# Kernel optimization log

Measured on AMD Instinct MI355X. Metric: run time of the kernel, lower is better.

Reference implementation:

```python
import jax, jax.numpy as jnp
import numpy as np

EPS = 1e-5  # BatchNorm eps

def gcn_conv(x, src, dst, n, W, b):
    # PyG GCNConv (normalize=True, add_self_loops=True):
    # out = D^{-1/2} (A + I) D^{-1/2} X W + b, messages aggregated at target (dst)
    deg = jax.ops.segment_sum(jnp.ones_like(dst, dtype=x.dtype), dst, num_segments=n)
    dinv = jnp.where(deg > 0, jax.lax.rsqrt(deg), 0.0)
    norm = dinv[src] * dinv[dst]                      # [E+N]
    xw = x @ W                                        # [N, out]
    out = jax.ops.segment_sum(norm[:, None] * xw[src], dst, num_segments=n)
    return out + b

def batch_norm(x, gamma, beta):
    # training-mode BatchNorm1d over node dim, biased variance
    mean = jnp.mean(x, axis=0)
    var = jnp.mean(jnp.square(x - mean), axis=0)
    return gamma * (x - mean) * jax.lax.rsqrt(var + EPS) + beta

def setup_inputs() -> dict:
    key = jax.random.key(0)
    ks = jax.random.split(key, 12)
    N, E, F_IN, DIM, F_OUT, L = 200000, 6400000, 64, 16, 16, 4
    x = jax.random.normal(ks[0], (N, F_IN), dtype=jnp.float32)
    edge_index = jax.random.randint(ks[1], (2, E), 0, N, dtype=jnp.int64)
    s = 0.1
    return {
        "x": x,
        "edge_index": edge_index,
        "W_in": jax.random.normal(ks[2], (F_IN, DIM), jnp.float32) * s,
        "b_in": jnp.zeros((DIM,), jnp.float32),
        "Ws": jax.random.normal(ks[3], (L, DIM, DIM), jnp.float32) * s,
        "bs": jnp.zeros((L, DIM), jnp.float32),
        "gammas": jnp.ones((L, DIM), jnp.float32),
        "betas": jnp.zeros((L, DIM), jnp.float32),
        "W_sin": jax.random.normal(ks[4], (DIM, F_OUT), jnp.float32) * s,
        "b_sin": jnp.zeros((F_OUT,), jnp.float32),
        "W_cos": jax.random.normal(ks[5], (DIM, F_OUT), jnp.float32) * s,
        "b_cos": jnp.zeros((F_OUT,), jnp.float32),
    }

def reference(x, edge_index, W_in, b_in, Ws, bs, gammas, betas, W_sin, b_sin, W_cos, b_cos):
    n = x.shape[0]
    loops = jnp.arange(n, dtype=edge_index.dtype)
    src = jnp.concatenate([edge_index[0], loops])   # add self loops once
    dst = jnp.concatenate([edge_index[1], loops])
    h = gcn_conv(x, src, dst, n, W_in, b_in)
    for l in range(Ws.shape[0]):
        h = gcn_conv(h, src, dst, n, Ws[l], bs[l])
        h = jax.nn.relu(batch_norm(h, gammas[l], betas[l]))
    sin_out = jax.nn.relu(gcn_conv(h, src, dst, n, W_sin, b_sin))
    cos_out = jax.nn.relu(gcn_conv(h, src, dst, n, W_cos, b_cos))
    return (sin_out, cos_out)
```

## Files before the change

kernel.cpp:

```cpp
#include <hip/hip_runtime.h>
#include <hip/hip_fp16.h>


#define DIM 16
#define F_IN 64
#define BUCK_SHIFT 10
#define BUCK_SIZE 1024
#define MAXB 256
#define HIST_CHUNK 4096
#define BIN_CHUNK 4096
#define EPB 16
#define CSR_CAP 33280

#define WA_OFF 0
#define WB_OFF 272
#define BA_OFF 544
#define BB_OFF 560
#define SW_SIZE 576
#define WIDX(f, j) ((f) * 17 + (j))


__global__ void hist_kernel(const int* __restrict__ dst, int* __restrict__ ghist,
                            int E, int nb) {
    __shared__ int lh[MAXB];
    int t = threadIdx.x;
    for (int i = t; i < nb; i += 256) lh[i] = 0;
    __syncthreads();
    int base = blockIdx.x * HIST_CHUNK;
    int end = min(base + HIST_CHUNK, E);
    for (int e = base + t; e < end; e += 256) atomicAdd(&lh[dst[e] >> BUCK_SHIFT], 1);
    __syncthreads();
    for (int b = t; b < nb; b += 256) {
        int c = lh[b];
        if (c) atomicAdd(&ghist[b], c);
    }
}

__global__ void scan_kernel(const int* __restrict__ ghist, int* __restrict__ boff,
                            int* __restrict__ cursor, int nb, int E) {
    __shared__ int sd[256];
    int t = threadIdx.x;
    int v = (t < nb) ? ghist[t] : 0;
    sd[t] = v;
    __syncthreads();
    for (int off = 1; off < 256; off <<= 1) {
        int u = (t >= off) ? sd[t - off] : 0;
        __syncthreads();
        sd[t] += u;
        __syncthreads();
    }
    if (t < nb) {
        int excl = sd[t] - v;
        boff[t] = excl;
        cursor[t] = excl;
    }
    if (t == 255) boff[nb] = E;
}

__launch_bounds__(256)
__global__ void bin_kernel(const int* __restrict__ src, const int* __restrict__ dst,
                           int* __restrict__ cursor, unsigned* __restrict__ packed,
                           int E, int nb) {
    __shared__ unsigned sedge[BIN_CHUNK];
    __shared__ unsigned char sbid[BIN_CHUNK];
    __shared__ int lh[MAXB];
    __shared__ int sd[MAXB];
    __shared__ int lstart[MAXB];
    __shared__ int lrank[MAXB];
    __shared__ int gbase[MAXB];

    int t = threadIdx.x;
    int base = blockIdx.x * BIN_CHUNK;
    int end = min(base + BIN_CHUNK, E);
    lh[t] = 0;
    __syncthreads();

    unsigned pv[EPB];
    int bk[EPB];
#pragma unroll
    for (int i = 0; i < EPB; ++i) {
        int e = base + t + i * 256;
        if (e < end) {
            int d = dst[e];
            int b = d >> BUCK_SHIFT;
            pv[i] = (unsigned)src[e] | ((unsigned)(d & (BUCK_SIZE - 1)) << 18);
            bk[i] = b;
            atomicAdd(&lh[b], 1);
        } else {
            bk[i] = -1;
            pv[i] = 0u;
        }
    }
    __syncthreads();

    int v = (t < nb) ? lh[t] : 0;
    sd[t] = v;
    __syncthreads();
    for (int off = 1; off < 256; off <<= 1) {
        int u = (t >= off) ? sd[t - off] : 0;
        __syncthreads();
        sd[t] += u;
        __syncthreads();
    }
    if (t < nb) {
        lstart[t] = sd[t] - v;
        lrank[t] = 0;
        gbase[t] = v ? atomicAdd(&cursor[t], v) : 0;
    }
    __syncthreads();

#pragma unroll
    for (int i = 0; i < EPB; ++i) {
        int b = bk[i];
        if (b >= 0) {
            int rank = atomicAdd(&lrank[b], 1);
            int p = lstart[b] + rank;
            sedge[p] = pv[i];
            sbid[p] = (unsigned char)b;
        }
    }
    __syncthreads();

    int total = end - base;
    for (int j = t; j < total; j += 256) {
        int b = sbid[j];
        packed[(size_t)gbase[b] + (unsigned)(j - lstart[b])] = sedge[j];
    }
}

__launch_bounds__(1024)
__global__ void csr_kernel(const unsigned* __restrict__ packed, const int* __restrict__ boff,
                           int* __restrict__ rowptr, float* __restrict__ dinv,
                           int* __restrict__ col, int N, int E) {
    extern __shared__ unsigned smem[];
    unsigned* sstage = smem;
    int* sd   = (int*)smem;
    int* cnt  = (int*)(smem + CSR_CAP);
    int* scur = cnt + BUCK_SIZE;

    int t = threadIdx.x, blk = blockIdx.x;
    cnt[t] = 0;
    __syncthreads();
    int b0 = boff[blk], e1 = boff[blk + 1];
    for (int e = b0 + t; e < e1; e += 1024) atomicAdd(&cnt[packed[e] >> 18], 1);
    __syncthreads();
    int d = cnt[t];
    sd[t] = d;
    __syncthreads();
    for (int off = 1; off < 1024; off <<= 1) {
        int v = (t >= off) ? sd[t - off] : 0;
        __syncthreads();
        sd[t] += v;
        __syncthreads();
    }
    int lstart = sd[t] - d;
    int i = (blk << BUCK_SHIFT) + t;
    if (i < N) {
        rowptr[i] = b0 + lstart;
        dinv[i] = rsqrtf((float)(d + 1));
        if (i == N - 1) rowptr[N] = E;
    }
    scur[t] = lstart;
    __syncthreads();
    for (int e = b0 + t; e < e1; e += 1024) {
        unsigned k = packed[e];
        int pos = atomicAdd(&scur[k >> 18], 1);
        unsigned val = k & 0x3FFFFu;
        if (pos < CSR_CAP) sstage[pos] = val;
        else col[(size_t)b0 + pos] = val;
    }
    __syncthreads();
    int total = e1 - b0;
    int lim = min(total, CSR_CAP);
    for (int j = t; j < lim; j += 1024) col[(size_t)b0 + j] = sstage[j];
}


__global__ void z0_kernel(const float* __restrict__ x, const float* __restrict__ W,
                          const float* __restrict__ dinv,
                          __half* __restrict__ z, int n) {
    __shared__ float sW[F_IN * DIM];
    int t = threadIdx.x;
#pragma unroll
    for (int j = 0; j < 4; ++j) sW[t + j * 256] = W[t + j * 256];
    __syncthreads();
    int idx = blockIdx.x * 256 + t;
    if (idx >= n * 2) return;
    int node = idx >> 1, p = idx & 1;
    float acc[8] = {0, 0, 0, 0, 0, 0, 0, 0};
    const float4* xr = (const float4*)(x + (size_t)node * F_IN);
#pragma unroll
    for (int k4 = 0; k4 < 16; ++k4) {
        float4 xv = xr[k4];
        float c[4] = { xv.x, xv.y, xv.z, xv.w };
#pragma unroll
        for (int cc = 0; cc < 4; ++cc) {
            const float* wr = &sW[(k4 * 4 + cc) * DIM + p * 8];
#pragma unroll
            for (int j = 0; j < 8; ++j) acc[j] += c[cc] * wr[j];
        }
    }
    float di = dinv[node];
    __half2 o[4];
#pragma unroll
    for (int m = 0; m < 4; ++m) o[m] = __floats2half2_rn(di * acc[2 * m], di * acc[2 * m + 1]);
    *(float4*)(z + ((size_t)node << 4) + p * 8) = *(float4*)o;
}

#define ACC_ROW(vl, vh)                                                        \
    {                                                                          \
        const __half2* hl_ = (const __half2*)&(vl);                            \
        const __half2* hh_ = (const __half2*)&(vh);                            \
        _Pragma("unroll")                                                      \
        for (int m_ = 0; m_ < 4; ++m_) {                                       \
            float2 f2_ = __half22float2(hl_[m_]);                              \
            a[2 * m_] += f2_.x; a[2 * m_ + 1] += f2_.y;                        \
            float2 g2_ = __half22float2(hh_[m_]);                              \
            a[8 + 2 * m_] += g2_.x; a[8 + 2 * m_ + 1] += g2_.y;                \
        }                                                                      \
    }


template <int MODE>
__launch_bounds__(256)
__global__ void gatherF_kernel(const int* __restrict__ rowptr, const int* __restrict__ col,
                               const __half* __restrict__ z, const float* __restrict__ dinv,
                               const float* __restrict__ Wa, const float* __restrict__ Wb,
                               const float* __restrict__ ba, const float* __restrict__ bb,
                               float* __restrict__ o1, float* __restrict__ o2,
                               __half* __restrict__ znext, float* __restrict__ bnsum, int N) {
    __shared__ float sW[SW_SIZE];
    __shared__ float sred[4][32];
    int t = threadIdx.x;
    if (MODE == 1 || MODE == 3) {
        int f = t >> 4, j = t & 15;
        sW[WA_OFF + WIDX(f, j)] = Wa[t];
        if (MODE == 3) sW[WB_OFF + WIDX(f, j)] = Wb[t];
        if (t < 16) {
            sW[BA_OFF + t] = ba[t];
            if (MODE == 3) sW[BB_OFF + t] = bb[t];
        }
        __syncthreads();
    } else {
        if (t < 16) sW[BA_OFF + t] = ba[t];
        __syncthreads();
    }

    int idx = blockIdx.x * 256 + t;
    int node = idx >> 3, o = idx & 7;
    bool alive = node < N;
    float a[16];
#pragma unroll
    for (int j = 0; j < 16; ++j) a[j] = 0.f;
    float di = 0.f;
    if (alive) {
        di = dinv[node];
        int start = rowptr[node];
        int len = rowptr[node + 1] - start;
        int k = o;
        for (; k + 24 < len; k += 32) {
            int s0 = col[start + k];
            int s1 = col[start + k + 8];
            int s2 = col[start + k + 16];
            int s3 = col[start + k + 24];
            const float4* q0 = (const float4*)(z + ((size_t)s0 << 4));
            const float4* q1 = (const float4*)(z + ((size_t)s1 << 4));
            const float4* q2 = (const float4*)(z + ((size_t)s2 << 4));
            const float4* q3 = (const float4*)(z + ((size_t)s3 << 4));
            float4 v0l = q0[0], v0h = q0[1];
            float4 v1l = q1[0], v1h = q1[1];
            float4 v2l = q2[0], v2h = q2[1];
            float4 v3l = q3[0], v3h = q3[1];
            ACC_ROW(v0l, v0h)
            ACC_ROW(v1l, v1h)
            ACC_ROW(v2l, v2h)
            ACC_ROW(v3l, v3h)
        }
        if (k + 8 < len) {
            int s0 = col[start + k];
            int s1 = col[start + k + 8];
            const float4* q0 = (const float4*)(z + ((size_t)s0 << 4));
            const float4* q1 = (const float4*)(z + ((size_t)s1 << 4));
            float4 v0l = q0[0], v0h = q0[1];
            float4 v1l = q1[0], v1h = q1[1];
            ACC_ROW(v0l, v0h)
            ACC_ROW(v1l, v1h)
            k += 16;
        }
        if (k < len) {
            int s = col[start + k];
            const float4* q = (const float4*)(z + ((size_t)s << 4));
            float4 vl = q[0], vh = q[1];
            ACC_ROW(vl, vh)
        }
    }
#pragma unroll
    for (int j = 0; j < 16; ++j) {
        a[j] += __shfl_xor(a[j], 1);
        a[j] += __shfl_xor(a[j], 2);
        a[j] += __shfl_xor(a[j], 4);
    }
    if (alive) {
        const float4* q = (const float4*)(z + ((size_t)node << 4));
        float4 vl = q[0], vh = q[1];
        ACC_ROW(vl, vh)
    }
    float r[16];
#pragma unroll
    for (int j = 0; j < 16; ++j) r[j] = di * a[j];

    if (MODE == 0) {
        if (alive && o == 0) {
            __half2 ov[8];
#pragma unroll
            for (int m = 0; m < 8; ++m)
                ov[m] = __floats2half2_rn(di * (r[2 * m] + sW[BA_OFF + 2 * m]),
                                          di * (r[2 * m + 1] + sW[BA_OFF + 2 * m + 1]));
            *(float4*)(znext + ((size_t)node << 4)) = ((float4*)ov)[0];
            *(float4*)(znext + ((size_t)node << 4) + 8) = ((float4*)ov)[1];
        }
        return;
    }

    float rc0 = 0.f, rc1 = 0.f;
#pragma unroll
    for (int j = 0; j < 8; ++j)
        if (o == j) { rc0 = r[2 * j]; rc1 = r[2 * j + 1]; }
    if (!alive) { rc0 = 0.f; rc1 = 0.f; }
    int f0 = 2 * o;
    float pa[16];
#pragma unroll
    for (int j = 0; j < 16; ++j)
        pa[j] = rc0 * sW[WA_OFF + WIDX(f0, j)] + rc1 * sW[WA_OFF + WIDX(f0 + 1, j)];
#pragma unroll
    for (int j = 0; j < 16; ++j) {
        pa[j] += __shfl_xor(pa[j], 1);
        pa[j] += __shfl_xor(pa[j], 2);
        pa[j] += __shfl_xor(pa[j], 4);
    }

    if (MODE == 1) {
        float o0 = 0.f, o1v = 0.f;
#pragma unroll
        for (int j = 0; j < 8; ++j)
            if (o == j) {
                o0 = pa[2 * j] + sW[BA_OFF + 2 * j];
                o1v = pa[2 * j + 1] + sW[BA_OFF + 2 * j + 1];
            }
        if (alive)
            *(float2*)(o1 + ((size_t)node << 4) + 2 * o) = make_float2(o0, o1v);
        float s0 = alive ? o0 : 0.f, s1 = alive ? o1v : 0.f;
        float q0 = s0 * s0, q1 = s1 * s1;
#pragma unroll
        for (int m = 8; m <= 32; m <<= 1) {
            s0 += __shfl_xor(s0, m); s1 += __shfl_xor(s1, m);
            q0 += __shfl_xor(q0, m); q1 += __shfl_xor(q1, m);
        }
        int lane = t & 63, wave = t >> 6;
        if (lane < 8) {
            sred[wave][2 * lane] = s0;
            sred[wave][2 * lane + 1] = s1;
            sred[wave][16 + 2 * lane] = q0;
            sred[wave][16 + 2 * lane + 1] = q1;
        }
        __syncthreads();
        if (t < 32) {
            float v = sred[0][t] + sred[1][t] + sred[2][t] + sred[3][t];
            atomicAdd(&bnsum[(blockIdx.x & 7) * 32 + t], v);
        }
        return;
    }

    {
        float pb[16];
#pragma unroll
        for (int j = 0; j < 16; ++j)
            pb[j] = rc0 * sW[WB_OFF + WIDX(f0, j)] + rc1 * sW[WB_OFF + WIDX(f0 + 1, j)];
#pragma unroll
        for (int j = 0; j < 16; ++j) {
            pb[j] += __shfl_xor(pb[j], 1);
            pb[j] += __shfl_xor(pb[j], 2);
            pb[j] += __shfl_xor(pb[j], 4);
        }
        if (alive) {
            float oa0 = 0.f, oa1 = 0.f, ob0 = 0.f, ob1 = 0.f;
#pragma unroll
            for (int j = 0; j < 8; ++j)
                if (o == j) {
                    oa0 = fmaxf(pa[2 * j] + sW[BA_OFF + 2 * j], 0.f);
                    oa1 = fmaxf(pa[2 * j + 1] + sW[BA_OFF + 2 * j + 1], 0.f);
                    ob0 = fmaxf(pb[2 * j] + sW[BB_OFF + 2 * j], 0.f);
                    ob1 = fmaxf(pb[2 * j + 1] + sW[BB_OFF + 2 * j + 1], 0.f);
                }
            *(float2*)(o1 + ((size_t)node << 4) + 2 * o) = make_float2(oa0, oa1);
            *(float2*)(o2 + ((size_t)node << 4) + 2 * o) = make_float2(ob0, ob1);
        }
    }
}


__global__ void bnfin_kernel(const float* __restrict__ bnsum, const float* __restrict__ gamma,
                             const float* __restrict__ beta, float* __restrict__ ssout, int n) {
    int t = threadIdx.x;
    if (t >= 16) return;
    float s = 0.f, sq = 0.f;
#pragma unroll
    for (int rep = 0; rep < 8; ++rep) {
        s += bnsum[rep * 32 + t];
        sq += bnsum[rep * 32 + 16 + t];
    }
    float invN = 1.f / (float)n;
    float mean = s * invN;
    float var = fmaxf(sq * invN - mean * mean, 0.f);
    float scale = gamma[t] * rsqrtf(var + 1e-5f);
    ssout[t] = scale;
    ssout[16 + t] = beta[t] - mean * scale;
}


__global__ void bn_relu_z_kernel(const float* __restrict__ hp, const float* __restrict__ ss,
                                 const float* __restrict__ dinv,
                                 __half* __restrict__ z, int n) {
    int idx = blockIdx.x * 256 + threadIdx.x;
    if (idx >= n * 2) return;
    int node = idx >> 1, p = idx & 1;
    float di = dinv[node];
    const float4* hr = (const float4*)(hp + ((size_t)node << 4) + p * 8);
    float4 v0 = hr[0], v1 = hr[1];
    float vv[8] = { v0.x, v0.y, v0.z, v0.w, v1.x, v1.y, v1.z, v1.w };
    __half2 o[4];
#pragma unroll
    for (int m = 0; m < 4; ++m) {
        int f0 = p * 8 + 2 * m;
        float r0 = di * fmaxf(vv[2 * m] * ss[f0] + ss[16 + f0], 0.f);
        float r1 = di * fmaxf(vv[2 * m + 1] * ss[f0 + 1] + ss[16 + f0 + 1], 0.f);
        o[m] = __floats2half2_rn(r0, r1);
    }
    *(float4*)(z + ((size_t)node << 4) + p * 8) = *(float4*)o;
}


extern "C" void kernel_launch(void* const* d_in, const int* in_sizes, int n_in,
                              void* d_out, int out_size, void* d_ws, size_t ws_size,
                              hipStream_t stream) {
    (void)n_in; (void)out_size; (void)ws_size;
    const float* x      = (const float*)d_in[0];
    const int*   edge   = (const int*)d_in[1];
    const float* W_in   = (const float*)d_in[2];
    const float* b_in   = (const float*)d_in[3];
    const float* Ws     = (const float*)d_in[4];
    const float* bs     = (const float*)d_in[5];
    const float* gammas = (const float*)d_in[6];
    const float* betas  = (const float*)d_in[7];
    const float* W_sin  = (const float*)d_in[8];
    const float* b_sin  = (const float*)d_in[9];
    const float* W_cos  = (const float*)d_in[10];
    const float* b_cos  = (const float*)d_in[11];
    float* out = (float*)d_out;

    const int N = in_sizes[0] / F_IN;
    const int E = in_sizes[1] / 2;
    const int L = in_sizes[4] / (DIM * DIM);
    const int nb = (N + BUCK_SIZE - 1) >> BUCK_SHIFT;
    const int* src = edge;
    const int* dst = edge + E;

    char* ws = (char*)d_ws;
    size_t off = 0;
    auto alloc = [&](size_t bytes) { char* p = ws + off; off += (bytes + 15) & ~size_t(15); return p; };
    float*    dinv   = (float*)alloc((size_t)N * 4);
    int*      ghist  = (int*)alloc((size_t)nb * 4);
    int*      boff   = (int*)alloc((size_t)(nb + 1) * 4);
    int*      cursor = (int*)alloc((size_t)nb * 4);
    int*      rowptr = (int*)alloc((size_t)(N + 1) * 4);
    unsigned* packed = (unsigned*)alloc((size_t)E * 4);
    int*      col    = (int*)alloc((size_t)E * 4);
    __half*   zA     = (__half*)alloc((size_t)N * 16 * 2);
    __half*   zB     = (__half*)alloc((size_t)N * 16 * 2);
    float*    hp     = (float*)alloc((size_t)N * DIM * 4);
    float*    bnsum  = (float*)alloc((size_t)L * 256 * 4);
    float*    ssbuf  = (float*)alloc((size_t)L * 32 * 4);

    hipMemsetAsync(ghist, 0, (size_t)nb * 4, stream);
    hipMemsetAsync(bnsum, 0, (size_t)L * 256 * 4, stream);

    const int nhist = (E + HIST_CHUNK - 1) / HIST_CHUNK;
    const int nbin  = (E + BIN_CHUNK - 1) / BIN_CHUNK;
    hist_kernel<<<nhist, 256, 0, stream>>>(dst, ghist, E, nb);
    scan_kernel<<<1, 256, 0, stream>>>(ghist, boff, cursor, nb, E);
    bin_kernel<<<nbin, 256, 0, stream>>>(src, dst, cursor, packed, E, nb);
    const size_t csr_lds = (size_t)(CSR_CAP + 2 * BUCK_SIZE) * 4;
    csr_kernel<<<nb, 1024, csr_lds, stream>>>(packed, boff, rowptr, dinv, col, N, E);

    const int G = (N * 8 + 255) / 256;

    z0_kernel<<<(N * 2 + 255) / 256, 256, 0, stream>>>(x, W_in, dinv, zA, N);
    gatherF_kernel<0><<<G, 256, 0, stream>>>(rowptr, col, zA, dinv,
                                             nullptr, nullptr, b_in, nullptr,
                                             nullptr, nullptr, zB, nullptr, N);
    __half* cur = zB;
    __half* nxt = zA;

    for (int l = 0; l < L; ++l) {
        gatherF_kernel<1><<<G, 256, 0, stream>>>(rowptr, col, cur, dinv,
                                                 Ws + l * DIM * DIM, nullptr,
                                                 bs + l * DIM, nullptr,
                                                 hp, nullptr, nullptr,
                                                 bnsum + l * 256, N);
        bnfin_kernel<<<1, 64, 0, stream>>>(bnsum + l * 256, gammas + l * DIM,
                                           betas + l * DIM, ssbuf + l * 32, N);
        bn_relu_z_kernel<<<(N * 2 + 255) / 256, 256, 0, stream>>>(hp, ssbuf + l * 32, dinv,
                                                                  nxt, N);
        __half* tz = cur; cur = nxt; nxt = tz;
    }

    gatherF_kernel<3><<<G, 256, 0, stream>>>(rowptr, col, cur, dinv,
                                             W_sin, W_cos, b_sin, b_cos,
                                             out, out + (size_t)N * DIM, nullptr,
                                             nullptr, N);
}
```

Baseline: 779.7 us.

## Split gather rows across thread pairs with 16 threads per node

The gather kernel now assigns 16 threads per node instead of 8. Each pair of threads splits a 16-half feature row into two 8-half halves, so every thread loads one float4 per neighbor and keeps 8 accumulators instead of 16. The dense transform is rewritten so each thread computes one output feature directly, after exchanging its partner's half, replacing the shuffle-reduced partial products. The intent is lower register pressure, higher occupancy and more memory parallelism. In exchange the grid doubles, the inner loop unrolls less (2 rows instead of 4 per iteration), and each random row fetch is split across two threads.

```diff
diff --git a/kernel.cpp b/kernel.cpp
--- a/kernel.cpp
+++ b/kernel.cpp
@@ -207,23 +207,21 @@
     *(float4*)(z + ((size_t)node << 4) + p * 8) = *(float4*)o;
 }
 
-#define ACC_ROW(vl, vh)                                                        \
+#define ACC8(v)                                                                \
     {                                                                          \
-        const __half2* hl_ = (const __half2*)&(vl);                            \
-        const __half2* hh_ = (const __half2*)&(vh);                            \
+        const __half2* h_ = (const __half2*)&(v);                              \
         _Pragma("unroll")                                                      \
         for (int m_ = 0; m_ < 4; ++m_) {                                       \
-            float2 f2_ = __half22float2(hl_[m_]);                              \
-            a[2 * m_] += f2_.x; a[2 * m_ + 1] += f2_.y;                        \
-            float2 g2_ = __half22float2(hh_[m_]);                              \
-            a[8 + 2 * m_] += g2_.x; a[8 + 2 * m_ + 1] += g2_.y;                \
+            float2 f_ = __half22float2(h_[m_]);                                \
+            a[2 * m_] += f_.x;                                                 \
+            a[2 * m_ + 1] += f_.y;                                             \
         }                                                                      \
     }
 
 
 template <int MODE>
 __launch_bounds__(256)
-__global__ void gatherF_kernel(const int* __restrict__ rowptr, const int* __restrict__ col,
+__global__ void gatherH_kernel(const int* __restrict__ rowptr, const int* __restrict__ col,
                                const __half* __restrict__ z, const float* __restrict__ dinv,
                                const float* __restrict__ Wa, const float* __restrict__ Wb,
                                const float* __restrict__ ba, const float* __restrict__ bb,
@@ -247,121 +245,84 @@
     }
 
     int idx = blockIdx.x * 256 + t;
-    int node = idx >> 3, o = idx & 7;
+    int node = idx >> 4, sub = idx & 15;
+    int par = sub & 1, slot = sub >> 1;
     bool alive = node < N;
-    float a[16];
-#pragma unroll
-    for (int j = 0; j < 16; ++j) a[j] = 0.f;
+    float a[8];
+#pragma unroll
+    for (int j = 0; j < 8; ++j) a[j] = 0.f;
     float di = 0.f;
     if (alive) {
         di = dinv[node];
         int start = rowptr[node];
         int len = rowptr[node + 1] - start;
-        int k = o;
-        for (; k + 24 < len; k += 32) {
+        int k = slot;
+        for (; k + 8 < len; k += 16) {
             int s0 = col[start + k];
             int s1 = col[start + k + 8];
-            int s2 = col[start + k + 16];
-            int s3 = col[start + k + 24];
-            const float4* q0 = (const float4*)(z + ((size_t)s0 << 4));
-            const float4* q1 = (const float4*)(z + ((size_t)s1 << 4));
-            const float4* q2 = (const float4*)(z + ((size_t)s2 << 4));
-            const float4* q3 = (const float4*)(z + ((size_t)s3 << 4));
-            float4 v0l = q0[0], v0h = q0[1];
-            float4 v1l = q1[0], v1h = q1[1];
-            float4 v2l = q2[0], v2h = q2[1];
-            float4 v3l = q3[0], v3h = q3[1];
-            ACC_ROW(v0l, v0h)
-            ACC_ROW(v1l, v1h)
-            ACC_ROW(v2l, v2h)
-            ACC_ROW(v3l, v3h)
-        }
-        if (k + 8 < len) {
-            int s0 = col[start + k];
-            int s1 = col[start + k + 8];
-            const float4* q0 = (const float4*)(z + ((size_t)s0 << 4));
-            const float4* q1 = (const float4*)(z + ((size_t)s1 << 4));
-            float4 v0l = q0[0], v0h = q0[1];
-            float4 v1l = q1[0], v1h = q1[1];
-            ACC_ROW(v0l, v0h)
-            ACC_ROW(v1l, v1h)
-            k += 16;
+            float4 v0 = *(const float4*)(z + ((size_t)s0 << 4) + par * 8);
+            float4 v1 = *(const float4*)(z + ((size_t)s1 << 4) + par * 8);
+            ACC8(v0)
+            ACC8(v1)
         }
         if (k < len) {
             int s = col[start + k];
-            const float4* q = (const float4*)(z + ((size_t)s << 4));
-            float4 vl = q[0], vh = q[1];
-            ACC_ROW(vl, vh)
-        }
-    }
-#pragma unroll
-    for (int j = 0; j < 16; ++j) {
-        a[j] += __shfl_xor(a[j], 1);
+            float4 v = *(const float4*)(z + ((size_t)s << 4) + par * 8);
+            ACC8(v)
+        }
+    }
+#pragma unroll
+    for (int j = 0; j < 8; ++j) {
         a[j] += __shfl_xor(a[j], 2);
         a[j] += __shfl_xor(a[j], 4);
+        a[j] += __shfl_xor(a[j], 8);
     }
     if (alive) {
-        const float4* q = (const float4*)(z + ((size_t)node << 4));
-        float4 vl = q[0], vh = q[1];
-        ACC_ROW(vl, vh)
-    }
-    float r[16];
-#pragma unroll
-    for (int j = 0; j < 16; ++j) r[j] = di * a[j];
+        float4 v = *(const float4*)(z + ((size_t)node << 4) + par * 8);
+        ACC8(v)
+    }
+    float r[8];
+#pragma unroll
+    for (int j = 0; j < 8; ++j) r[j] = di * a[j];
 
     if (MODE == 0) {
-        if (alive && o == 0) {
-            __half2 ov[8];
-#pragma unroll
-            for (int m = 0; m < 8; ++m)
-                ov[m] = __floats2half2_rn(di * (r[2 * m] + sW[BA_OFF + 2 * m]),
-                                          di * (r[2 * m + 1] + sW[BA_OFF + 2 * m + 1]));
-            *(float4*)(znext + ((size_t)node << 4)) = ((float4*)ov)[0];
-            *(float4*)(znext + ((size_t)node << 4) + 8) = ((float4*)ov)[1];
+        if (alive && slot == 0) {
+            __half2 ov[4];
+#pragma unroll
+            for (int m = 0; m < 4; ++m) {
+                int f = par * 8 + 2 * m;
+                ov[m] = __floats2half2_rn(di * (r[2 * m] + sW[BA_OFF + f]),
+                                          di * (r[2 * m + 1] + sW[BA_OFF + f + 1]));
+            }
+            *(float4*)(znext + ((size_t)node << 4) + par * 8) = *(float4*)ov;
         }
         return;
     }
 
-    float rc0 = 0.f, rc1 = 0.f;
-#pragma unroll
-    for (int j = 0; j < 8; ++j)
-        if (o == j) { rc0 = r[2 * j]; rc1 = r[2 * j + 1]; }
-    if (!alive) { rc0 = 0.f; rc1 = 0.f; }
-    int f0 = 2 * o;
-    float pa[16];
-#pragma unroll
-    for (int j = 0; j < 16; ++j)
-        pa[j] = rc0 * sW[WA_OFF + WIDX(f0, j)] + rc1 * sW[WA_OFF + WIDX(f0 + 1, j)];
-#pragma unroll
-    for (int j = 0; j < 16; ++j) {
-        pa[j] += __shfl_xor(pa[j], 1);
-        pa[j] += __shfl_xor(pa[j], 2);
-        pa[j] += __shfl_xor(pa[j], 4);
-    }
+    float xv[8];
+#pragma unroll
+    for (int j = 0; j < 8; ++j) xv[j] = __shfl_xor(r[j], 1);
+    float rf[16];
+#pragma unroll
+    for (int f = 0; f < 8; ++f) {
+        rf[f] = par ? xv[f] : r[f];
+        rf[8 + f] = par ? r[f] : xv[f];
+    }
+    int j = sub;
+    float oa = sW[BA_OFF + j];
+#pragma unroll
+    for (int f = 0; f < 16; ++f) oa += rf[f] * sW[WA_OFF + WIDX(f, j)];
 
     if (MODE == 1) {
-        float o0 = 0.f, o1v = 0.f;
-#pragma unroll
-        for (int j = 0; j < 8; ++j)
-            if (o == j) {
-                o0 = pa[2 * j] + sW[BA_OFF + 2 * j];
-                o1v = pa[2 * j + 1] + sW[BA_OFF + 2 * j + 1];
-            }
-        if (alive)
-            *(float2*)(o1 + ((size_t)node << 4) + 2 * o) = make_float2(o0, o1v);
-        float s0 = alive ? o0 : 0.f, s1 = alive ? o1v : 0.f;
-        float q0 = s0 * s0, q1 = s1 * s1;
-#pragma unroll
-        for (int m = 8; m <= 32; m <<= 1) {
-            s0 += __shfl_xor(s0, m); s1 += __shfl_xor(s1, m);
-            q0 += __shfl_xor(q0, m); q1 += __shfl_xor(q1, m);
-        }
+        if (alive) o1[((size_t)node << 4) + j] = oa;
+        float s0 = alive ? oa : 0.f;
+        float q0 = s0 * s0;
+        s0 += __shfl_xor(s0, 16); q0 += __shfl_xor(q0, 16);
+        s0 += __shfl_xor(s0, 32); q0 += __shfl_xor(q0, 32);
         int lane = t & 63, wave = t >> 6;
-        if (lane < 8) {
-            sred[wave][2 * lane] = s0;
-            sred[wave][2 * lane + 1] = s1;
-            sred[wave][16 + 2 * lane] = q0;
-            sred[wave][16 + 2 * lane + 1] = q1;
+        if (lane < 16) {
+            sred[wave][lane] = s0;
+            sred[wave][16 + lane] = q0;
         }
         __syncthreads();
         if (t < 32) {
@@ -372,28 +333,12 @@
     }
 
     {
-        float pb[16];
-#pragma unroll
-        for (int j = 0; j < 16; ++j)
-            pb[j] = rc0 * sW[WB_OFF + WIDX(f0, j)] + rc1 * sW[WB_OFF + WIDX(f0 + 1, j)];
-#pragma unroll
-        for (int j = 0; j < 16; ++j) {
-            pb[j] += __shfl_xor(pb[j], 1);
-            pb[j] += __shfl_xor(pb[j], 2);
-            pb[j] += __shfl_xor(pb[j], 4);
-        }
+        float ob = sW[BB_OFF + j];
+#pragma unroll
+        for (int f = 0; f < 16; ++f) ob += rf[f] * sW[WB_OFF + WIDX(f, j)];
         if (alive) {
-            float oa0 = 0.f, oa1 = 0.f, ob0 = 0.f, ob1 = 0.f;
-#pragma unroll
-            for (int j = 0; j < 8; ++j)
-                if (o == j) {
-                    oa0 = fmaxf(pa[2 * j] + sW[BA_OFF + 2 * j], 0.f);
-                    oa1 = fmaxf(pa[2 * j + 1] + sW[BA_OFF + 2 * j + 1], 0.f);
-                    ob0 = fmaxf(pb[2 * j] + sW[BB_OFF + 2 * j], 0.f);
-                    ob1 = fmaxf(pb[2 * j + 1] + sW[BB_OFF + 2 * j + 1], 0.f);
-                }
-            *(float2*)(o1 + ((size_t)node << 4) + 2 * o) = make_float2(oa0, oa1);
-            *(float2*)(o2 + ((size_t)node << 4) + 2 * o) = make_float2(ob0, ob1);
+            o1[((size_t)node << 4) + j] = fmaxf(oa, 0.f);
+            o2[((size_t)node << 4) + j] = fmaxf(ob, 0.f);
         }
     }
 }
@@ -492,21 +437,21 @@
     const size_t csr_lds = (size_t)(CSR_CAP + 2 * BUCK_SIZE) * 4;
     csr_kernel<<<nb, 1024, csr_lds, stream>>>(packed, boff, rowptr, dinv, col, N, E);
 
-    const int G = (N * 8 + 255) / 256;
+    const int G16 = (N * 16 + 255) / 256;
 
     z0_kernel<<<(N * 2 + 255) / 256, 256, 0, stream>>>(x, W_in, dinv, zA, N);
-    gatherF_kernel<0><<<G, 256, 0, stream>>>(rowptr, col, zA, dinv,
-                                             nullptr, nullptr, b_in, nullptr,
-                                             nullptr, nullptr, zB, nullptr, N);
+    gatherH_kernel<0><<<G16, 256, 0, stream>>>(rowptr, col, zA, dinv,
+                                               nullptr, nullptr, b_in, nullptr,
+                                               nullptr, nullptr, zB, nullptr, N);
     __half* cur = zB;
     __half* nxt = zA;
 
     for (int l = 0; l < L; ++l) {
-        gatherF_kernel<1><<<G, 256, 0, stream>>>(rowptr, col, cur, dinv,
-                                                 Ws + l * DIM * DIM, nullptr,
-                                                 bs + l * DIM, nullptr,
-                                                 hp, nullptr, nullptr,
-                                                 bnsum + l * 256, N);
+        gatherH_kernel<1><<<G16, 256, 0, stream>>>(rowptr, col, cur, dinv,
+                                                   Ws + l * DIM * DIM, nullptr,
+                                                   bs + l * DIM, nullptr,
+                                                   hp, nullptr, nullptr,
+                                                   bnsum + l * 256, N);
         bnfin_kernel<<<1, 64, 0, stream>>>(bnsum + l * 256, gammas + l * DIM,
                                            betas + l * DIM, ssbuf + l * 32, N);
         bn_relu_z_kernel<<<(N * 2 + 255) / 256, 256, 0, stream>>>(hp, ssbuf + l * 32, dinv,
@@ -514,8 +459,8 @@
         __half* tz = cur; cur = nxt; nxt = tz;
     }
 
-    gatherF_kernel<3><<<G, 256, 0, stream>>>(rowptr, col, cur, dinv,
-                                             W_sin, W_cos, b_sin, b_cos,
-                                             out, out + (size_t)N * DIM, nullptr,
-                                             nullptr, N);
-}
+    gatherH_kernel<3><<<G16, 256, 0, stream>>>(rowptr, col, cur, dinv,
+                                               W_sin, W_cos, b_sin, b_cos,
+                                               out, out + (size_t)N * DIM, nullptr,
+                                               nullptr, N);
+}
```

Result: slower. 802.6 us (+2.9%).
